# Kernel tuning notes

Hardware: AMD Instinct MI355X
Metric: run time of the kernel (lower is better)

The kernel has to match this reference:

```python
import jax, jax.numpy as jnp
import numpy as np

B = 131072
EPS = 1e-5

def _attn(x, Wq, Wk, Wv, Wo):
    # x: (B, 10, 1); Wq/Wk/Wv: (1, 16); Wo: (16, 1)
    Q = x @ Wq  # (B, 10, 16)
    K = x @ Wk
    V = x @ Wv
    A = jnp.einsum('bqd,bkd->bqk', Q, K) / 4.0  # sqrt(16) = 4
    A = jax.nn.softmax(A, axis=1)  # NOTE: torch Softmax(dim=1) -> axis 1, not -1
    out = jnp.einsum('bqk,bkd->bqd', A, V) @ Wo  # (B, 10, 1)
    return out[..., 0]  # squeeze -> (B, 10)

def _bn(h, gamma, beta):
    # BatchNorm1d training-mode math (batch stats, biased variance)
    mu = jnp.mean(h, axis=0)
    var = jnp.mean(jnp.square(h - mu), axis=0)
    return gamma * (h - mu) * jax.lax.rsqrt(var + EPS) + beta

def setup_inputs() -> dict:
    key = jax.random.key(0)
    ks = jax.random.split(key, 24)
    n = lambda k, shp, s=1.0: (jax.random.normal(k, shp, dtype=jnp.float32) * s)
    inp = {
        'x':   n(ks[0], (B, 10, 1)),
        'Wq1': n(ks[1], (1, 16)), 'Wk1': n(ks[2], (1, 16)),
        'Wv1': n(ks[3], (1, 16)), 'Wo1': n(ks[4], (16, 1)),
        'Wq2': n(ks[5], (1, 16)), 'Wk2': n(ks[6], (1, 16)),
        'Wv2': n(ks[7], (1, 16)), 'Wo2': n(ks[8], (16, 1)),
        # layer1: Linear(10,128) BN ReLU Linear(128,256) BN ReLU Linear(256,10)
        'W1a': n(ks[9], (10, 128), 0.3), 'b1a': jnp.zeros((128,), jnp.float32),
        'g1a': jnp.ones((128,), jnp.float32), 'be1a': jnp.zeros((128,), jnp.float32),
        'W1b': n(ks[10], (128, 256), 0.09), 'b1b': jnp.zeros((256,), jnp.float32),
        'g1b': jnp.ones((256,), jnp.float32), 'be1b': jnp.zeros((256,), jnp.float32),
        'W1c': n(ks[11], (256, 10), 0.06), 'b1c': jnp.zeros((10,), jnp.float32),
        # layer2: Linear(10,128) BN ReLU Linear(128,256) BN ReLU Linear(256,2)
        'W2a': n(ks[12], (10, 128), 0.3), 'b2a': jnp.zeros((128,), jnp.float32),
        'g2a': jnp.ones((128,), jnp.float32), 'be2a': jnp.zeros((128,), jnp.float32),
        'W2b': n(ks[13], (128, 256), 0.09), 'b2b': jnp.zeros((256,), jnp.float32),
        'g2b': jnp.ones((256,), jnp.float32), 'be2b': jnp.zeros((256,), jnp.float32),
        'W2c': n(ks[14], (256, 2), 0.06), 'b2c': jnp.zeros((2,), jnp.float32),
    }
    return inp

def reference(x, Wq1, Wk1, Wv1, Wo1, Wq2, Wk2, Wv2, Wo2,
              W1a, b1a, g1a, be1a, W1b, b1b, g1b, be1b, W1c, b1c,
              W2a, b2a, g2a, be2a, W2b, b2b, g2b, be2b, W2c, b2c):
    h = _attn(x, Wq1, Wk1, Wv1, Wo1)                 # (B, 10)
    h = jax.nn.relu(_bn(h @ W1a + b1a, g1a, be1a))   # (B, 128)
    h = jax.nn.relu(_bn(h @ W1b + b1b, g1b, be1b))   # (B, 256)
    h = h @ W1c + b1c                                # (B, 10)
    h = _attn(h[..., None], Wq2, Wk2, Wv2, Wo2)      # (B, 10)
    h = jax.nn.relu(_bn(h @ W2a + b2a, g2a, be2a))   # (B, 128)
    h = jax.nn.relu(_bn(h @ W2b + b2b, g2b, be2b))   # (B, 256)
    return h @ W2c + b2c                             # (B, 2)
```

## Files before the change

kernel.cpp:

```cpp
#include <hip/hip_runtime.h>
#include <hip/hip_bf16.h>

#define EPS 1e-5f
constexpr int BN = 131072;
constexpr int NBKT = 32;

typedef __attribute__((ext_vector_type(8))) short bf16x8;
typedef __attribute__((ext_vector_type(4))) float f32x4;

constexpr size_t OFF_H   = 0;
constexpr size_t OFF_HH  = OFF_H  + (size_t)BN*10;
constexpr size_t OFF_M1  = OFF_HH + (size_t)BN*10;
constexpr size_t OFF_S2  = OFF_M1 + 65;
constexpr size_t OFF_M3  = OFF_S2 + 512;
constexpr size_t OFF_S4  = OFF_M3 + 65;
constexpr size_t OFF_WA1 = OFF_S4 + 512;
constexpr size_t OFF_BA1 = OFF_WA1 + 1280;
constexpr size_t OFF_WA2 = OFF_BA1 + 128;
constexpr size_t OFF_BA2 = OFF_WA2 + 1280;
constexpr size_t OFF_SC2 = OFF_BA2 + 128;
constexpr size_t OFF_TC2 = OFF_SC2 + 256;
constexpr size_t OFF_SC4 = OFF_TC2 + 256;
constexpr size_t OFF_TC4 = OFF_SC4 + 256;
constexpr size_t OFF_WB1 = OFF_TC4 + 256;
constexpr size_t OFF_BB1 = OFF_WB1 + 32768;
constexpr size_t OFF_WB2 = OFF_BB1 + 256;
constexpr size_t OFF_BB2 = OFF_WB2 + 32768;
constexpr size_t OFF_P1  = OFF_BB2 + 256;
constexpr size_t OFF_P3  = OFF_P1 + 1024*65;
constexpr size_t OFF_S2B = OFF_P3 + 1024*65;
constexpr size_t OFF_S4B = OFF_S2B + (size_t)NBKT*512;
constexpr size_t OFF_WT1 = OFF_S4B + (size_t)NBKT*512;
constexpr size_t OFF_WT2 = OFF_WT1 + 16384;
constexpr size_t OFF_END = OFF_WT2 + 16384;
constexpr size_t OFF_Z_BYTES = ((OFF_END*4 + 255) & ~(size_t)255);
constexpr size_t WS_NEED = OFF_Z_BYTES + (size_t)256*BN*2;

__device__ __forceinline__ float wsum(float v){
  v += __shfl_down(v, 32);
  v += __shfl_down(v, 16);
  v += __shfl_down(v, 8);
  v += __shfl_down(v, 4);
  v += __shfl_down(v, 2);
  v += __shfl_down(v, 1);
  return v;
}

__device__ __forceinline__ unsigned pk_bf16(float a, float b){
  union { __hip_bfloat16 h[2]; unsigned u; } cv;
  cv.h[0] = __float2bfloat16(a);
  cv.h[1] = __float2bfloat16(b);
  return cv.u;
}

__device__ __forceinline__ unsigned short bf16_1(float a){
  union { __hip_bfloat16 h; unsigned short u; } cv;
  cv.h = __float2bfloat16(a);
  return cv.u;
}

__device__ __forceinline__ float bf16_to_f(unsigned short u){
  return __uint_as_float(((unsigned)u) << 16);
}

__device__ __forceinline__ void attn10(const float* xr, float cqk, float cvo, float* y){
  #pragma unroll
  for (int q=0;q<10;q++) y[q] = 0.f;
  #pragma unroll
  for (int k=0;k<10;k++){
    float t = cqk * xr[k];
    float m = t*xr[0];
    #pragma unroll
    for (int q=1;q<10;q++) m = fmaxf(m, t*xr[q]);
    float ex[10]; float s = 0.f;
    #pragma unroll
    for (int q=0;q<10;q++){ ex[q] = __expf(t*xr[q]-m); s += ex[q]; }
    float f = xr[k]/s;
    #pragma unroll
    for (int q=0;q<10;q++) y[q] += ex[q]*f;
  }
  #pragma unroll
  for (int q=0;q<10;q++) y[q] *= cvo;
}

__device__ __forceinline__ void moments_block(const float* y, float (*red)[65],
                                              float* Pb, int t){
  int lane = t & 63, w = t >> 6;
  #pragma unroll
  for (int i=0;i<10;i++){
    float v = wsum(y[i]);
    if (lane==0) red[w][i] = v;
  }
  #pragma unroll
  for (int i=0;i<10;i++){
    #pragma unroll
    for (int j=i;j<10;j++){
      float v = wsum(y[i]*y[j]);
      if (lane==0) red[w][10 + 10*i - i*(i-1)/2 + (j-i)] = v;
    }
  }
  __syncthreads();
  if (t < 65)
    Pb[(size_t)blockIdx.x*65 + t] = red[0][t]+red[1][t]+red[2][t]+red[3][t];
}

__device__ __forceinline__ void moments10(const float* y, float* M, int lane){
  #pragma unroll
  for (int i=0;i<10;i++){
    float s = wsum(y[i]);
    if (lane==0) atomicAdd(&M[i], s);
  }
  #pragma unroll
  for (int i=0;i<10;i++){
    #pragma unroll
    for (int j=i;j<10;j++){
      int id = 10*i - i*(i-1)/2 + (j-i);
      float s = wsum(y[i]*y[j]);
      if (lane==0) atomicAdd(&M[10+id], s);
    }
  }
}

__global__ __launch_bounds__(256) void k_attn_in(
    const float* __restrict__ x,
    const float* __restrict__ Wq, const float* __restrict__ Wk,
    const float* __restrict__ Wv, const float* __restrict__ Wo,
    float* __restrict__ h, float* __restrict__ Pb){
  __shared__ float xs[256][11];
  __shared__ float red[4][65];
  int t = threadIdx.x;
  size_t base = (size_t)blockIdx.x*2560;
  for (int idx=t; idx<2560; idx+=256) xs[idx/10][idx%10] = x[base+idx];
  float cqk=0.f, cvo=0.f;
  #pragma unroll
  for (int d=0;d<16;d++){ cqk += Wq[d]*Wk[d]; cvo += Wv[d]*Wo[d]; }
  cqk *= 0.25f;
  __syncthreads();
  float xr[10];
  #pragma unroll
  for (int q=0;q<10;q++) xr[q] = xs[t][q];
  float y[10];
  attn10(xr, cqk, cvo, y);
  #pragma unroll
  for (int q=0;q<10;q++) xs[t][q] = y[q];
  moments_block(y, red, Pb, t);
  for (int idx=t; idx<2560; idx+=256) h[base+idx] = xs[idx/10][idx%10];
}

__global__ void k_fold10_part(const float* __restrict__ Pb, int npart,
                              const float* __restrict__ W,
                              const float* __restrict__ bv, const float* __restrict__ g,
                              const float* __restrict__ be,
                              float* __restrict__ WT, float* __restrict__ bo){
  __shared__ float part[65][8];
  __shared__ float sM[65];
  int t = threadIdx.x;
  if (t < 520){
    int c = t>>3, k = t&7;
    int n = npart>>3;
    float acc = 0.f;
    #pragma unroll 4
    for (int i=0;i<n;i++) acc += Pb[(size_t)(k*n+i)*65 + c];
    part[c][k] = acc;
  }
  __syncthreads();
  if (t < 65){
    float a = 0.f;
    #pragma unroll
    for (int k=0;k<8;k++) a += part[t][k];
    sM[t] = a;
  }
  __syncthreads();
  int j = t;
  if (j >= 128) return;
  const float invB = 1.f/(float)BN;
  float Eh[10];
  #pragma unroll
  for (int i=0;i<10;i++) Eh[i] = sM[i]*invB;
  float wj[10];
  #pragma unroll
  for (int i=0;i<10;i++) wj[i] = W[i*128+j];
  float mu = bv[j];
  #pragma unroll
  for (int i=0;i<10;i++) mu += Eh[i]*wj[i];
  float var = 0.f;
  #pragma unroll
  for (int i=0;i<10;i++){
    #pragma unroll
    for (int l=0;l<10;l++){
      int a = i<l ? i : l, c = i<l ? l : i;
      int id = 10*a - a*(a-1)/2 + (c-a);
      float cov = sM[10+id]*invB - Eh[i]*Eh[l];
      var += wj[i]*wj[l]*cov;
    }
  }
  float s = g[j]*rsqrtf(var + EPS);
  #pragma unroll
  for (int i=0;i<10;i++) WT[j*10+i] = wj[i]*s;
  bo[j] = (bv[j]-mu)*s + be[j];
}

__global__ void k_fold10_atomic(const float* __restrict__ M,
                                const float* __restrict__ W,
                                const float* __restrict__ bv, const float* __restrict__ g,
                                const float* __restrict__ be,
                                float* __restrict__ WT, float* __restrict__ bo){
  int j = threadIdx.x;
  if (j >= 128) return;
  const float invB = 1.f/(float)BN;
  float Eh[10];
  #pragma unroll
  for (int i=0;i<10;i++) Eh[i] = M[i]*invB;
  float wj[10];
  #pragma unroll
  for (int i=0;i<10;i++) wj[i] = W[i*128+j];
  float mu = bv[j];
  #pragma unroll
  for (int i=0;i<10;i++) mu += Eh[i]*wj[i];
  float var = 0.f;
  #pragma unroll
  for (int i=0;i<10;i++){
    #pragma unroll
    for (int l=0;l<10;l++){
      int a = i<l ? i : l, c = i<l ? l : i;
      int id = 10*a - a*(a-1)/2 + (c-a);
      float cov = M[10+id]*invB - Eh[i]*Eh[l];
      var += wj[i]*wj[l]*cov;
    }
  }
  float s = g[j]*rsqrtf(var + EPS);
  #pragma unroll
  for (int i=0;i<10;i++) WT[j*10+i] = wj[i]*s;
  bo[j] = (bv[j]-mu)*s + be[j];
}

__global__ void k_fold_affine(const float* __restrict__ stats,
                              const float* __restrict__ g,
                              const float* __restrict__ be,
                              float* __restrict__ s, float* __restrict__ tt){
  int j = threadIdx.x;
  if (j >= 256) return;
  float su = 0.f, sq = 0.f;
  #pragma unroll 4
  for (int k=0;k<NBKT;k++){
    su += stats[k*512 + j];
    sq += stats[k*512 + 256 + j];
  }
  const float invB = 1.f/(float)BN;
  float mu  = su*invB;
  float var = sq*invB - mu*mu;
  float sc = g[j]*rsqrtf(var + EPS);
  s[j]  = sc;
  tt[j] = be[j] - mu*sc;
}

__global__ __launch_bounds__(256) void k_prep_wt2(
    const float* __restrict__ W1, const float* __restrict__ W2,
    unsigned short* __restrict__ WT1, unsigned short* __restrict__ WT2){
  int g = blockIdx.x;
  const float* W = (g < 128) ? W1 : W2;
  unsigned short* WT = (g < 128) ? WT1 : WT2;
  int idx = (g & 127)*256 + threadIdx.x;
  int c = idx >> 7, k = idx & 127;
  WT[idx] = bf16_1(W[k*256 + c]);
}

__device__ __forceinline__ void block_gemm(
    const float* __restrict__ h, const float* __restrict__ WaT,
    const float* __restrict__ ba, const unsigned short* __restrict__ WT,
    unsigned short* h1s, float (*hs)[11], float* sWaT,
    f32x4 (&acc)[4][4], int t, size_t row0)
{
  int lane = t & 63, w = t >> 6;
  int ci = lane & 15, g = lane >> 4;

  bf16x8 bfr[4][4];
  #pragma unroll
  for (int nt=0; nt<4; nt++)
    #pragma unroll
    for (int kt=0; kt<4; kt++){
      union { uint4 u; bf16x8 v; } cv;
      cv.u = *(const uint4*)(WT + (size_t)(w*64 + nt*16 + ci)*128 + kt*32 + g*8);
      bfr[nt][kt] = cv.v;
    }

  for (int idx = t; idx < 640; idx += 256) hs[idx/10][idx%10] = h[row0*10 + idx];
  for (int idx = t; idx < 1280; idx += 256) sWaT[idx] = WaT[idx];
  __syncthreads();

  {
    int r = lane;
    int i0 = w * 32;
    float hr[10];
    #pragma unroll
    for (int l=0;l<10;l++) hr[l] = hs[r][l];
    #pragma unroll
    for (int j=0;j<4;j++){
      unsigned pk[4];
      #pragma unroll
      for (int q=0;q<4;q++){
        int i = i0 + j*8 + q*2;
        float v0 = ba[i], v1 = ba[i+1];
        #pragma unroll
        for (int l=0;l<10;l++){
          v0 = fmaf(hr[l], sWaT[i*10+l],     v0);
          v1 = fmaf(hr[l], sWaT[(i+1)*10+l], v1);
        }
        pk[q] = pk_bf16(fmaxf(v0,0.f), fmaxf(v1,0.f));
      }
      int byte = r*256 + (((i0 + j*8)*2) ^ ((r&7)<<4));
      *(uint4*)((char*)h1s + byte) = make_uint4(pk[0],pk[1],pk[2],pk[3]);
    }
  }
  __syncthreads();

  #pragma unroll
  for (int mt=0;mt<4;mt++)
    #pragma unroll
    for (int nt=0;nt<4;nt++)
      acc[mt][nt] = (f32x4){0.f,0.f,0.f,0.f};

  #pragma unroll
  for (int mt=0; mt<4; mt++){
    int r = mt*16 + ci;
    bf16x8 af[4];
    #pragma unroll
    for (int kt=0; kt<4; kt++){
      int byte = r*256 + ((kt*64 + g*16) ^ ((r&7)<<4));
      af[kt] = *(const bf16x8*)((const char*)h1s + byte);
    }
    #pragma unroll
    for (int nt=0; nt<4; nt++)
      #pragma unroll
      for (int kt=0; kt<4; kt++)
        acc[mt][nt] = __builtin_amdgcn_mfma_f32_16x16x32_bf16(
            af[kt], bfr[nt][kt], acc[mt][nt], 0, 0, 0);
  }
}

__global__ __launch_bounds__(256) void k_layer_mfma(
    const float* __restrict__ h,
    const float* __restrict__ WaT,
    const float* __restrict__ ba,
    const unsigned short* __restrict__ WT,
    const float* __restrict__ bb,
    unsigned short* __restrict__ zt,
    float* __restrict__ stats)
{
  __shared__ __align__(16) char smem[36864];
  unsigned short* h1s = (unsigned short*)smem;
  float (*hs)[11]     = (float(*)[11])(smem + 16384);
  float* sWaT         = (float*)(smem + 19200);
  unsigned short* zs  = (unsigned short*)smem;
  int t = threadIdx.x;
  int lane = t & 63, w = t >> 6;
  int ci = lane & 15, g = lane >> 4;
  size_t row0 = (size_t)blockIdx.x * 64;

  f32x4 acc[4][4];
  block_gemm(h, WaT, ba, WT, h1s, hs, sWaT, acc, t, row0);

  float bbv[4];
  #pragma unroll
  for (int nt=0;nt<4;nt++) bbv[nt] = bb[w*64 + nt*16 + ci];
  float s1v[4], s2v[4];
  #pragma unroll
  for (int nt=0; nt<4; nt++){
    float cs = 0.f, cq = 0.f;
    #pragma unroll
    for (int mt=0; mt<4; mt++)
      #pragma unroll
      for (int j=0;j<4;j++){
        float zv = acc[mt][nt][j] + bbv[nt];
        acc[mt][nt][j] = zv;
        cs += zv;
        cq += zv*zv;
      }
    cs += __shfl_down(cs, 32); cs += __shfl_down(cs, 16);
    cq += __shfl_down(cq, 32); cq += __shfl_down(cq, 16);
    s1v[nt] = cs; s2v[nt] = cq;
  }
  __syncthreads();

  #pragma unroll
  for (int mt=0; mt<4; mt++)
    #pragma unroll
    for (int nt=0; nt<4; nt++){
      int c = w*64 + nt*16 + ci;
      int r0 = mt*16 + g*4;
      uint2 v;
      v.x = pk_bf16(acc[mt][nt][0], acc[mt][nt][1]);
      v.y = pk_bf16(acc[mt][nt][2], acc[mt][nt][3]);
      *(uint2*)&zs[c*72 + r0] = v;
    }
  __syncthreads();

  #pragma unroll
  for (int pass=0; pass<8; pass++){
    int c  = (t>>3) + pass*32;
    int rc = (t&7)*8;
    uint4 v = *(const uint4*)&zs[c*72 + rc];
    *(uint4*)(zt + (size_t)c*BN + row0 + rc) = v;
  }

  if (lane < 16){
    int bkt = blockIdx.x & (NBKT-1);
    #pragma unroll
    for (int nt=0; nt<4; nt++){
      int c = w*64 + nt*16 + ci;
      atomicAdd(&stats[bkt*512 + c],       s1v[nt]);
      atomicAdd(&stats[bkt*512 + 256 + c], s2v[nt]);
    }
  }
}

__global__ __launch_bounds__(256) void k_consume_mid(
    const unsigned short* __restrict__ zt,
    const float* __restrict__ s_g, const float* __restrict__ t_g,
    const float* __restrict__ Wc,  const float* __restrict__ bc,
    const float* __restrict__ Wq, const float* __restrict__ Wk,
    const float* __restrict__ Wv, const float* __restrict__ Wo,
    float* __restrict__ hh, float* __restrict__ Pb){
  __shared__ __align__(16) unsigned short zs[32*256];
  __shared__ __align__(16) float sWc[256*12];
  __shared__ float ss[256], st[256];
  __shared__ float red[4][65];
  int t = threadIdx.x;
  for (int idx=t; idx<2560; idx+=256) sWc[(idx/10)*12 + (idx%10)] = Wc[idx];
  ss[t] = s_g[t]; st[t] = t_g[t];
  size_t b0 = (size_t)blockIdx.x*256;

  float z3[10];
  #pragma unroll
  for (int l=0;l<10;l++) z3[l] = bc[l];

  int c8 = t >> 3, i8 = t & 7;
  for (int cc=0; cc<8; cc++){
    __syncthreads();
    {
      int c = cc*32 + c8;
      const uint4* src = (const uint4*)(zt + (size_t)c*BN + b0 + i8*32);
      uint4* dst = (uint4*)&zs[c8*256 + i8*32];
      dst[0] = src[0]; dst[1] = src[1]; dst[2] = src[2]; dst[3] = src[3];
    }
    __syncthreads();
    #pragma unroll 4
    for (int cl=0; cl<32; cl++){
      int c = cc*32 + cl;
      float f = bf16_to_f(zs[cl*256 + t]);
      float h2 = fmaxf(fmaf(ss[c], f, st[c]), 0.f);
      const float4* wr = (const float4*)&sWc[c*12];
      float4 w0 = wr[0];
      float4 w1 = wr[1];
      float2 w2 = *(const float2*)&sWc[c*12 + 8];
      z3[0] = fmaf(h2, w0.x, z3[0]); z3[1] = fmaf(h2, w0.y, z3[1]);
      z3[2] = fmaf(h2, w0.z, z3[2]); z3[3] = fmaf(h2, w0.w, z3[3]);
      z3[4] = fmaf(h2, w1.x, z3[4]); z3[5] = fmaf(h2, w1.y, z3[5]);
      z3[6] = fmaf(h2, w1.z, z3[6]); z3[7] = fmaf(h2, w1.w, z3[7]);
      z3[8] = fmaf(h2, w2.x, z3[8]); z3[9] = fmaf(h2, w2.y, z3[9]);
    }
  }

  float cqk=0.f, cvo=0.f;
  #pragma unroll
  for (int d=0;d<16;d++){ cqk += Wq[d]*Wk[d]; cvo += Wv[d]*Wo[d]; }
  cqk *= 0.25f;
  float y[10];
  attn10(z3, cqk, cvo, y);
  __syncthreads();
  float* hhs = (float*)zs;
  #pragma unroll
  for (int q=0;q<10;q++) hhs[t*10+q] = y[q];
  moments_block(y, red, Pb, t);
  for (int idx=t; idx<2560; idx+=256)
    hh[b0*10 + idx] = hhs[idx];
}

__global__ __launch_bounds__(256) void k_consume_out(
    const unsigned short* __restrict__ zt,
    const float* __restrict__ s_g, const float* __restrict__ t_g,
    const float* __restrict__ Wc,  const float* __restrict__ bc,
    float* __restrict__ out){
  __shared__ __align__(16) unsigned short zs[32*256];
  __shared__ __align__(8) float sWo[512];
  __shared__ float ss[256], st[256];
  int t = threadIdx.x;
  sWo[t] = Wc[t]; sWo[256+t] = Wc[256+t];
  ss[t] = s_g[t]; st[t] = t_g[t];
  size_t b0 = (size_t)blockIdx.x*256;
  float o0 = bc[0], o1 = bc[1];
  int c8 = t >> 3, i8 = t & 7;
  for (int cc=0; cc<8; cc++){
    __syncthreads();
    {
      int c = cc*32 + c8;
      const uint4* src = (const uint4*)(zt + (size_t)c*BN + b0 + i8*32);
      uint4* dst = (uint4*)&zs[c8*256 + i8*32];
      dst[0] = src[0]; dst[1] = src[1]; dst[2] = src[2]; dst[3] = src[3];
    }
    __syncthreads();
    #pragma unroll 8
    for (int cl=0; cl<32; cl++){
      int c = cc*32 + cl;
      float f = bf16_to_f(zs[cl*256 + t]);
      float h5 = fmaxf(fmaf(ss[c], f, st[c]), 0.f);
      float2 wv = *(const float2*)&sWo[c*2];
      o0 = fmaf(h5, wv.x, o0);
      o1 = fmaf(h5, wv.y, o1);
    }
  }
  *(float2*)(out + (b0 + t)*2) = make_float2(o0, o1);
}

__global__ void k_fold_big(const float* __restrict__ stats,
                           const float* __restrict__ W,
                           const float* __restrict__ bv, const float* __restrict__ g,
                           const float* __restrict__ be,
                           float* __restrict__ Wf, float* __restrict__ bf){
  int j = blockIdx.x*256 + threadIdx.x;
  if (j >= 256) return;
  const float invB = 1.f/(float)BN;
  float mu  = stats[j]*invB;
  float var = stats[256+j]*invB - mu*mu;
  float s = g[j]*rsqrtf(var + EPS);
  bf[j] = (bv[j]-mu)*s + be[j];
  for (int i=0;i<128;i++) Wf[i*256+j] = W[i*256+j]*s;
}

__global__ __launch_bounds__(256) void k_mid(
    const float* __restrict__ h,
    const float* __restrict__ WaT, const float* __restrict__ ba,
    const float* __restrict__ Wb,  const float* __restrict__ bb,
    float* __restrict__ stats){
  int b = blockIdx.x*256 + threadIdx.x;
  if (b >= BN) return;
  float hr[10];
  #pragma unroll
  for (int l=0;l<10;l++) hr[l] = h[(size_t)b*10+l];
  int lane = threadIdx.x & 63;
  for (int jc=0;jc<4;jc++){
    float acc[64];
    #pragma unroll
    for (int j=0;j<64;j++) acc[j] = bb[jc*64+j];
    for (int i=0;i<128;i++){
      float h1 = ba[i];
      #pragma unroll
      for (int l=0;l<10;l++) h1 += hr[l]*WaT[i*10+l];
      h1 = fmaxf(h1, 0.f);
      const float* __restrict__ w = &Wb[i*256 + jc*64];
      #pragma unroll
      for (int j=0;j<64;j++) acc[j] += h1*w[j];
    }
    #pragma unroll
    for (int j=0;j<64;j++){
      float s1 = wsum(acc[j]);
      float s2 = wsum(acc[j]*acc[j]);
      if (lane==0){
        atomicAdd(&stats[jc*64+j], s1);
        atomicAdd(&stats[256+jc*64+j], s2);
      }
    }
  }
}

__global__ __launch_bounds__(256) void k_mid2(
    const float* __restrict__ h,
    const float* __restrict__ WaT, const float* __restrict__ ba,
    const float* __restrict__ Wbf, const float* __restrict__ bbf,
    const float* __restrict__ Wc,  const float* __restrict__ bc,
    const float* __restrict__ Wq, const float* __restrict__ Wk,
    const float* __restrict__ Wv, const float* __restrict__ Wo,
    float* __restrict__ hh, float* __restrict__ M){
  int b = blockIdx.x*256 + threadIdx.x;
  if (b >= BN) return;
  float hr[10];
  #pragma unroll
  for (int l=0;l<10;l++) hr[l] = h[(size_t)b*10+l];
  float z3[10];
  #pragma unroll
  for (int l=0;l<10;l++) z3[l] = bc[l];
  for (int jc=0;jc<4;jc++){
    float acc[64];
    #pragma unroll
    for (int j=0;j<64;j++) acc[j] = bbf[jc*64+j];
    for (int i=0;i<128;i++){
      float h1 = ba[i];
      #pragma unroll
      for (int l=0;l<10;l++) h1 += hr[l]*WaT[i*10+l];
      h1 = fmaxf(h1, 0.f);
      const float* __restrict__ w = &Wbf[i*256 + jc*64];
      #pragma unroll
      for (int j=0;j<64;j++) acc[j] += h1*w[j];
    }
    #pragma unroll
    for (int j=0;j<64;j++){
      float h2 = fmaxf(acc[j], 0.f);
      const float* __restrict__ wc = &Wc[(jc*64+j)*10];
      #pragma unroll
      for (int l=0;l<10;l++) z3[l] += h2*wc[l];
    }
  }
  float cqk=0.f, cvo=0.f;
  #pragma unroll
  for (int d=0;d<16;d++){ cqk += Wq[d]*Wk[d]; cvo += Wv[d]*Wo[d]; }
  cqk *= 0.25f;
  float y[10];
  attn10(z3, cqk, cvo, y);
  #pragma unroll
  for (int q=0;q<10;q++) hh[(size_t)b*10+q] = y[q];
  moments10(y, M, threadIdx.x & 63);
}

__global__ __launch_bounds__(256) void k_out(
    const float* __restrict__ h,
    const float* __restrict__ WaT, const float* __restrict__ ba,
    const float* __restrict__ Wbf, const float* __restrict__ bbf,
    const float* __restrict__ Wc,  const float* __restrict__ bc,
    float* __restrict__ out){
  int b = blockIdx.x*256 + threadIdx.x;
  if (b >= BN) return;
  float hr[10];
  #pragma unroll
  for (int l=0;l<10;l++) hr[l] = h[(size_t)b*10+l];
  float o0 = bc[0], o1 = bc[1];
  for (int jc=0;jc<4;jc++){
    float acc[64];
    #pragma unroll
    for (int j=0;j<64;j++) acc[j] = bbf[jc*64+j];
    for (int i=0;i<128;i++){
      float h4 = ba[i];
      #pragma unroll
      for (int l=0;l<10;l++) h4 += hr[l]*WaT[i*10+l];
      h4 = fmaxf(h4, 0.f);
      const float* __restrict__ w = &Wbf[i*256 + jc*64];
      #pragma unroll
      for (int j=0;j<64;j++) acc[j] += h4*w[j];
    }
    #pragma unroll
    for (int j=0;j<64;j++){
      float h5 = fmaxf(acc[j], 0.f);
      o0 += h5*Wc[(jc*64+j)*2];
      o1 += h5*Wc[(jc*64+j)*2+1];
    }
  }
  out[(size_t)b*2]   = o0;
  out[(size_t)b*2+1] = o1;
}

extern "C" void kernel_launch(void* const* d_in, const int* in_sizes, int n_in,
                              void* d_out, int out_size, void* d_ws, size_t ws_size,
                              hipStream_t stream){
  const float* x   = (const float*)d_in[0];
  const float* Wq1 = (const float*)d_in[1];
  const float* Wk1 = (const float*)d_in[2];
  const float* Wv1 = (const float*)d_in[3];
  const float* Wo1 = (const float*)d_in[4];
  const float* Wq2 = (const float*)d_in[5];
  const float* Wk2 = (const float*)d_in[6];
  const float* Wv2 = (const float*)d_in[7];
  const float* Wo2 = (const float*)d_in[8];
  const float* W1a = (const float*)d_in[9];  const float* b1a = (const float*)d_in[10];
  const float* g1a = (const float*)d_in[11]; const float* be1a= (const float*)d_in[12];
  const float* W1b = (const float*)d_in[13]; const float* b1b = (const float*)d_in[14];
  const float* g1b = (const float*)d_in[15]; const float* be1b= (const float*)d_in[16];
  const float* W1c = (const float*)d_in[17]; const float* b1c = (const float*)d_in[18];
  const float* W2a = (const float*)d_in[19]; const float* b2a = (const float*)d_in[20];
  const float* g2a = (const float*)d_in[21]; const float* be2a= (const float*)d_in[22];
  const float* W2b = (const float*)d_in[23]; const float* b2b = (const float*)d_in[24];
  const float* g2b = (const float*)d_in[25]; const float* be2b= (const float*)d_in[26];
  const float* W2c = (const float*)d_in[27]; const float* b2c = (const float*)d_in[28];

  float* f   = (float*)d_ws;
  float* h   = f + OFF_H;
  float* hh  = f + OFF_HH;
  float* M1  = f + OFF_M1;
  float* S2  = f + OFF_S2;
  float* M3  = f + OFF_M3;
  float* S4  = f + OFF_S4;
  float* WA1 = f + OFF_WA1; float* BA1 = f + OFF_BA1;
  float* WA2 = f + OFF_WA2; float* BA2 = f + OFF_BA2;
  float* SC2 = f + OFF_SC2; float* TC2 = f + OFF_TC2;
  float* SC4 = f + OFF_SC4; float* TC4 = f + OFF_TC4;
  float* WB1 = f + OFF_WB1; float* BB1 = f + OFF_BB1;
  float* WB2 = f + OFF_WB2; float* BB2 = f + OFF_BB2;
  float* P1  = f + OFF_P1;  float* P3  = f + OFF_P3;
  float* S2B = f + OFF_S2B; float* S4B = f + OFF_S4B;
  unsigned short* WT1 = (unsigned short*)(f + OFF_WT1);
  unsigned short* WT2 = (unsigned short*)(f + OFF_WT2);
  unsigned short* ZT = (unsigned short*)((char*)d_ws + OFF_Z_BYTES);

  dim3 blk(256);
  dim3 grid256(BN/256);
  dim3 grid64(BN/64);

  if (ws_size >= WS_NEED){
    hipMemsetAsync(S2B, 0, (size_t)2*NBKT*512*sizeof(float), stream);
    k_prep_wt2<<<256,blk,0,stream>>>(W1b, W2b, WT1, WT2);
    k_attn_in<<<grid256,blk,0,stream>>>(x, Wq1,Wk1,Wv1,Wo1, h, P1);
    k_fold10_part<<<1,576,0,stream>>>(P1, 512, W1a,b1a,g1a,be1a, WA1,BA1);
    k_layer_mfma<<<grid64,blk,0,stream>>>(h, WA1,BA1, WT1,b1b, ZT, S2B);
    k_fold_affine<<<1,256,0,stream>>>(S2B, g1b, be1b, SC2, TC2);
    k_consume_mid<<<grid256,blk,0,stream>>>(ZT, SC2,TC2, W1c,b1c,
                                            Wq2,Wk2,Wv2,Wo2, hh, P3);
    k_fold10_part<<<1,576,0,stream>>>(P3, 512, W2a,b2a,g2a,be2a, WA2,BA2);
    k_layer_mfma<<<grid64,blk,0,stream>>>(hh, WA2,BA2, WT2,b2b, ZT, S4B);
    k_fold_affine<<<1,256,0,stream>>>(S4B, g2b, be2b, SC4, TC4);
    k_consume_out<<<grid256,blk,0,stream>>>(ZT, SC4,TC4, W2c,b2c, (float*)d_out);
  } else {
    hipMemsetAsync(M1, 0, (65+512+65+512)*sizeof(float), stream);
    k_attn_in<<<grid256,blk,0,stream>>>(x, Wq1,Wk1,Wv1,Wo1, h, P1);
    k_fold10_part<<<1,576,0,stream>>>(P1, 512, W1a,b1a,g1a,be1a, WA1,BA1);
    k_mid<<<grid256,blk,0,stream>>>(h, WA1,BA1, W1b,b1b, S2);
    k_fold_big<<<1,256,0,stream>>>(S2, W1b,b1b,g1b,be1b, WB1,BB1);
    k_mid2<<<grid256,blk,0,stream>>>(h, WA1,BA1, WB1,BB1, W1c,b1c,
                                     Wq2,Wk2,Wv2,Wo2, hh, M3);
    k_fold10_atomic<<<1,128,0,stream>>>(M3, W2a,b2a,g2a,be2a, WA2,BA2);
    k_mid<<<grid256,blk,0,stream>>>(hh, WA2,BA2, W2b,b2b, S4);
    k_fold_big<<<1,256,0,stream>>>(S4, W2b,b2b,g2b,be2b, WB2,BB2);
    k_out<<<grid256,blk,0,stream>>>(hh, WA2,BA2, WB2,BB2, W2c,b2c, (float*)d_out);
  }
}
```

Baseline: 218.5 us.

## Double-buffer z tile loads in consumer kernels and pad z row stride

The consumer kernels now prefetch the next 32-channel chunk of the transposed bf16 activation into registers while computing on the current chunk. The chunk is written into an alternate shared-memory buffer, which removes one barrier per iteration and overlaps global loads with FMA work. The z row stride is also padded from BN to BN+64 elements to avoid channel-aligned address aliasing across rows. The cost is doubled LDS use for zs and a slightly larger workspace, which may lower occupancy.

```diff
diff --git a/kernel.cpp b/kernel.cpp
--- a/kernel.cpp
+++ b/kernel.cpp
@@ -4,6 +4,7 @@
 #define EPS 1e-5f
 constexpr int BN = 131072;
 constexpr int NBKT = 32;
+constexpr int ZLD = BN + 64;
 
 typedef __attribute__((ext_vector_type(8))) short bf16x8;
 typedef __attribute__((ext_vector_type(4))) float f32x4;
@@ -34,7 +35,7 @@
 constexpr size_t OFF_WT2 = OFF_WT1 + 16384;
 constexpr size_t OFF_END = OFF_WT2 + 16384;
 constexpr size_t OFF_Z_BYTES = ((OFF_END*4 + 255) & ~(size_t)255);
-constexpr size_t WS_NEED = OFF_Z_BYTES + (size_t)256*BN*2;
+constexpr size_t WS_NEED = OFF_Z_BYTES + (size_t)256*ZLD*2;
 
 __device__ __forceinline__ float wsum(float v){
   v += __shfl_down(v, 32);
@@ -400,7 +401,7 @@
     int c  = (t>>3) + pass*32;
     int rc = (t&7)*8;
     uint4 v = *(const uint4*)&zs[c*72 + rc];
-    *(uint4*)(zt + (size_t)c*BN + row0 + rc) = v;
+    *(uint4*)(zt + (size_t)c*ZLD + row0 + rc) = v;
   }
 
   if (lane < 16){
@@ -421,7 +422,7 @@
     const float* __restrict__ Wq, const float* __restrict__ Wk,
     const float* __restrict__ Wv, const float* __restrict__ Wo,
     float* __restrict__ hh, float* __restrict__ Pb){
-  __shared__ __align__(16) unsigned short zs[32*256];
+  __shared__ __align__(16) unsigned short zs[2][32*256];
   __shared__ __align__(16) float sWc[256*12];
   __shared__ float ss[256], st[256];
   __shared__ float red[4][65];
@@ -435,19 +436,25 @@
   for (int l=0;l<10;l++) z3[l] = bc[l];
 
   int c8 = t >> 3, i8 = t & 7;
+  uint4 r0, r1, r2, r3;
+  {
+    const uint4* src = (const uint4*)(zt + (size_t)c8*ZLD + b0 + i8*32);
+    r0 = src[0]; r1 = src[1]; r2 = src[2]; r3 = src[3];
+    uint4* dst = (uint4*)&zs[0][c8*256 + i8*32];
+    dst[0] = r0; dst[1] = r1; dst[2] = r2; dst[3] = r3;
+  }
   for (int cc=0; cc<8; cc++){
     __syncthreads();
-    {
-      int c = cc*32 + c8;
-      const uint4* src = (const uint4*)(zt + (size_t)c*BN + b0 + i8*32);
-      uint4* dst = (uint4*)&zs[c8*256 + i8*32];
-      dst[0] = src[0]; dst[1] = src[1]; dst[2] = src[2]; dst[3] = src[3];
-    }
-    __syncthreads();
+    if (cc < 7){
+      int c = (cc+1)*32 + c8;
+      const uint4* src = (const uint4*)(zt + (size_t)c*ZLD + b0 + i8*32);
+      r0 = src[0]; r1 = src[1]; r2 = src[2]; r3 = src[3];
+    }
+    const unsigned short* zb = zs[cc&1];
     #pragma unroll 4
     for (int cl=0; cl<32; cl++){
       int c = cc*32 + cl;
-      float f = bf16_to_f(zs[cl*256 + t]);
+      float f = bf16_to_f(zb[cl*256 + t]);
       float h2 = fmaxf(fmaf(ss[c], f, st[c]), 0.f);
       const float4* wr = (const float4*)&sWc[c*12];
       float4 w0 = wr[0];
@@ -459,6 +466,10 @@
       z3[6] = fmaf(h2, w1.z, z3[6]); z3[7] = fmaf(h2, w1.w, z3[7]);
       z3[8] = fmaf(h2, w2.x, z3[8]); z3[9] = fmaf(h2, w2.y, z3[9]);
     }
+    if (cc < 7){
+      uint4* dst = (uint4*)&zs[(cc+1)&1][c8*256 + i8*32];
+      dst[0] = r0; dst[1] = r1; dst[2] = r2; dst[3] = r3;
+    }
   }
 
   float cqk=0.f, cvo=0.f;
@@ -468,7 +479,7 @@
   float y[10];
   attn10(z3, cqk, cvo, y);
   __syncthreads();
-  float* hhs = (float*)zs;
+  float* hhs = (float*)zs[0];
   #pragma unroll
   for (int q=0;q<10;q++) hhs[t*10+q] = y[q];
   moments_block(y, red, Pb, t);
@@ -481,7 +492,7 @@
     const float* __restrict__ s_g, const float* __restrict__ t_g,
     const float* __restrict__ Wc,  const float* __restrict__ bc,
     float* __restrict__ out){
-  __shared__ __align__(16) unsigned short zs[32*256];
+  __shared__ __align__(16) unsigned short zs[2][32*256];
   __shared__ __align__(8) float sWo[512];
   __shared__ float ss[256], st[256];
   int t = threadIdx.x;
@@ -490,23 +501,33 @@
   size_t b0 = (size_t)blockIdx.x*256;
   float o0 = bc[0], o1 = bc[1];
   int c8 = t >> 3, i8 = t & 7;
+  uint4 r0, r1, r2, r3;
+  {
+    const uint4* src = (const uint4*)(zt + (size_t)c8*ZLD + b0 + i8*32);
+    r0 = src[0]; r1 = src[1]; r2 = src[2]; r3 = src[3];
+    uint4* dst = (uint4*)&zs[0][c8*256 + i8*32];
+    dst[0] = r0; dst[1] = r1; dst[2] = r2; dst[3] = r3;
+  }
   for (int cc=0; cc<8; cc++){
     __syncthreads();
-    {
-      int c = cc*32 + c8;
-      const uint4* src = (const uint4*)(zt + (size_t)c*BN + b0 + i8*32);
-      uint4* dst = (uint4*)&zs[c8*256 + i8*32];
-      dst[0] = src[0]; dst[1] = src[1]; dst[2] = src[2]; dst[3] = src[3];
-    }
-    __syncthreads();
+    if (cc < 7){
+      int c = (cc+1)*32 + c8;
+      const uint4* src = (const uint4*)(zt + (size_t)c*ZLD + b0 + i8*32);
+      r0 = src[0]; r1 = src[1]; r2 = src[2]; r3 = src[3];
+    }
+    const unsigned short* zb = zs[cc&1];
     #pragma unroll 8
     for (int cl=0; cl<32; cl++){
       int c = cc*32 + cl;
-      float f = bf16_to_f(zs[cl*256 + t]);
+      float f = bf16_to_f(zb[cl*256 + t]);
       float h5 = fmaxf(fmaf(ss[c], f, st[c]), 0.f);
       float2 wv = *(const float2*)&sWo[c*2];
       o0 = fmaf(h5, wv.x, o0);
       o1 = fmaf(h5, wv.y, o1);
+    }
+    if (cc < 7){
+      uint4* dst = (uint4*)&zs[(cc+1)&1][c8*256 + i8*32];
+      dst[0] = r0; dst[1] = r1; dst[2] = r2; dst[3] = r3;
     }
   }
   *(float2*)(out + (b0 + t)*2) = make_float2(o0, o1);
```

Result: no change. 217.1 us (-0.6%).

## Store intermediate Z row-major and use MFMA for small output projections

Applied to the files above, without the earlier changes.

The layer kernel now writes the bf16 pre-BN activations row-major (B x 256) directly from accumulators instead of staging a transposed column-major layout through shared memory. The consume kernels switch to 64-row blocks that load contiguous rows into swizzled LDS, apply BN+ReLU in place, and compute the 256->10 and 256->2 projections with bf16 MFMA using pre-packed padded weights, produced by a new prep kernel. Partial moment buffers grow to match the larger grid. The direct scattered 2-byte global stores from the layer kernel may be poorly coalesced, and the projection inputs are now rounded to bf16.

```diff
diff --git a/kernel.cpp b/kernel.cpp
--- a/kernel.cpp
+++ b/kernel.cpp
@@ -27,14 +27,16 @@
 constexpr size_t OFF_WB2 = OFF_BB1 + 256;
 constexpr size_t OFF_BB2 = OFF_WB2 + 32768;
 constexpr size_t OFF_P1  = OFF_BB2 + 256;
-constexpr size_t OFF_P3  = OFF_P1 + 1024*65;
-constexpr size_t OFF_S2B = OFF_P3 + 1024*65;
+constexpr size_t OFF_P3  = OFF_P1 + 512*65;
+constexpr size_t OFF_S2B = OFF_P3 + (size_t)2048*65;
 constexpr size_t OFF_S4B = OFF_S2B + (size_t)NBKT*512;
 constexpr size_t OFF_WT1 = OFF_S4B + (size_t)NBKT*512;
 constexpr size_t OFF_WT2 = OFF_WT1 + 16384;
-constexpr size_t OFF_END = OFF_WT2 + 16384;
+constexpr size_t OFF_WCP = OFF_WT2 + 16384;
+constexpr size_t OFF_WOP = OFF_WCP + 2048;
+constexpr size_t OFF_END = OFF_WOP + 2048;
 constexpr size_t OFF_Z_BYTES = ((OFF_END*4 + 255) & ~(size_t)255);
-constexpr size_t WS_NEED = OFF_Z_BYTES + (size_t)256*BN*2;
+constexpr size_t WS_NEED = OFF_Z_BYTES + (size_t)BN*256*2;
 
 __device__ __forceinline__ float wsum(float v){
   v += __shfl_down(v, 32);
@@ -59,9 +61,8 @@
   return cv.u;
 }
 
-__device__ __forceinline__ float bf16_to_f(unsigned short u){
-  return __uint_as_float(((unsigned)u) << 16);
-}
+__device__ __forceinline__ float bf16_lo(unsigned u){ return __uint_as_float(u << 16); }
+__device__ __forceinline__ float bf16_hi(unsigned u){ return __uint_as_float(u & 0xffff0000u); }
 
 __device__ __forceinline__ void attn10(const float* xr, float cqk, float cvo, float* y){
   #pragma unroll
@@ -265,6 +266,20 @@
   WT[idx] = bf16_1(W[k*256 + c]);
 }
 
+__global__ void k_prep_wcp(const float* __restrict__ W1c, const float* __restrict__ W2c,
+                           unsigned short* __restrict__ WcP,
+                           unsigned short* __restrict__ WoP){
+  int t = threadIdx.x;
+  int lane = t & 63;
+  int q = lane & 15;
+  int kb = (t>>6)*32 + (lane>>4)*8;
+  #pragma unroll
+  for (int e=0;e<8;e++){
+    WcP[t*8+e] = (q<10) ? bf16_1(W1c[(kb+e)*10 + q]) : (unsigned short)0;
+    WoP[t*8+e] = (q<2)  ? bf16_1(W2c[(kb+e)*2  + q]) : (unsigned short)0;
+  }
+}
+
 __device__ __forceinline__ void block_gemm(
     const float* __restrict__ h, const float* __restrict__ WaT,
     const float* __restrict__ ba, const unsigned short* __restrict__ WT,
@@ -344,14 +359,12 @@
     const float* __restrict__ ba,
     const unsigned short* __restrict__ WT,
     const float* __restrict__ bb,
-    unsigned short* __restrict__ zt,
+    unsigned short* __restrict__ z,
     float* __restrict__ stats)
 {
-  __shared__ __align__(16) char smem[36864];
-  unsigned short* h1s = (unsigned short*)smem;
-  float (*hs)[11]     = (float(*)[11])(smem + 16384);
-  float* sWaT         = (float*)(smem + 19200);
-  unsigned short* zs  = (unsigned short*)smem;
+  __shared__ unsigned short h1s[64*128];
+  __shared__ float hs[64][11];
+  __shared__ float sWaT[1280];
   int t = threadIdx.x;
   int lane = t & 63, w = t >> 6;
   int ci = lane & 15, g = lane >> 4;
@@ -367,12 +380,14 @@
   #pragma unroll
   for (int nt=0; nt<4; nt++){
     float cs = 0.f, cq = 0.f;
+    int c = w*64 + nt*16 + ci;
     #pragma unroll
     for (int mt=0; mt<4; mt++)
       #pragma unroll
       for (int j=0;j<4;j++){
         float zv = acc[mt][nt][j] + bbv[nt];
-        acc[mt][nt][j] = zv;
+        int r = mt*16 + g*4 + j;
+        z[(row0 + r)*256 + c] = bf16_1(zv);
         cs += zv;
         cq += zv*zv;
       }
@@ -380,29 +395,6 @@
     cq += __shfl_down(cq, 32); cq += __shfl_down(cq, 16);
     s1v[nt] = cs; s2v[nt] = cq;
   }
-  __syncthreads();
-
-  #pragma unroll
-  for (int mt=0; mt<4; mt++)
-    #pragma unroll
-    for (int nt=0; nt<4; nt++){
-      int c = w*64 + nt*16 + ci;
-      int r0 = mt*16 + g*4;
-      uint2 v;
-      v.x = pk_bf16(acc[mt][nt][0], acc[mt][nt][1]);
-      v.y = pk_bf16(acc[mt][nt][2], acc[mt][nt][3]);
-      *(uint2*)&zs[c*72 + r0] = v;
-    }
-  __syncthreads();
-
-  #pragma unroll
-  for (int pass=0; pass<8; pass++){
-    int c  = (t>>3) + pass*32;
-    int rc = (t&7)*8;
-    uint4 v = *(const uint4*)&zs[c*72 + rc];
-    *(uint4*)(zt + (size_t)c*BN + row0 + rc) = v;
-  }
-
   if (lane < 16){
     int bkt = blockIdx.x & (NBKT-1);
     #pragma unroll
@@ -415,101 +407,196 @@
 }
 
 __global__ __launch_bounds__(256) void k_consume_mid(
-    const unsigned short* __restrict__ zt,
+    const unsigned short* __restrict__ z,
     const float* __restrict__ s_g, const float* __restrict__ t_g,
-    const float* __restrict__ Wc,  const float* __restrict__ bc,
+    const unsigned short* __restrict__ WcP, const float* __restrict__ bc,
     const float* __restrict__ Wq, const float* __restrict__ Wk,
     const float* __restrict__ Wv, const float* __restrict__ Wo,
     float* __restrict__ hh, float* __restrict__ Pb){
-  __shared__ __align__(16) unsigned short zs[32*256];
-  __shared__ __align__(16) float sWc[256*12];
+  __shared__ __align__(16) unsigned short zs[64*256];
   __shared__ float ss[256], st[256];
-  __shared__ float red[4][65];
+  __shared__ float z3s[64][10];
   int t = threadIdx.x;
-  for (int idx=t; idx<2560; idx+=256) sWc[(idx/10)*12 + (idx%10)] = Wc[idx];
+  int lane = t & 63, w = t >> 6;
+  int ci = lane & 15, g = lane >> 4;
+  size_t row0 = (size_t)blockIdx.x * 64;
+
   ss[t] = s_g[t]; st[t] = t_g[t];
-  size_t b0 = (size_t)blockIdx.x*256;
-
-  float z3[10];
-  #pragma unroll
-  for (int l=0;l<10;l++) z3[l] = bc[l];
-
-  int c8 = t >> 3, i8 = t & 7;
-  for (int cc=0; cc<8; cc++){
-    __syncthreads();
-    {
-      int c = cc*32 + c8;
-      const uint4* src = (const uint4*)(zt + (size_t)c*BN + b0 + i8*32);
-      uint4* dst = (uint4*)&zs[c8*256 + i8*32];
-      dst[0] = src[0]; dst[1] = src[1]; dst[2] = src[2]; dst[3] = src[3];
-    }
-    __syncthreads();
-    #pragma unroll 4
-    for (int cl=0; cl<32; cl++){
-      int c = cc*32 + cl;
-      float f = bf16_to_f(zs[cl*256 + t]);
-      float h2 = fmaxf(fmaf(ss[c], f, st[c]), 0.f);
-      const float4* wr = (const float4*)&sWc[c*12];
-      float4 w0 = wr[0];
-      float4 w1 = wr[1];
-      float2 w2 = *(const float2*)&sWc[c*12 + 8];
-      z3[0] = fmaf(h2, w0.x, z3[0]); z3[1] = fmaf(h2, w0.y, z3[1]);
-      z3[2] = fmaf(h2, w0.z, z3[2]); z3[3] = fmaf(h2, w0.w, z3[3]);
-      z3[4] = fmaf(h2, w1.x, z3[4]); z3[5] = fmaf(h2, w1.y, z3[5]);
-      z3[6] = fmaf(h2, w1.z, z3[6]); z3[7] = fmaf(h2, w1.w, z3[7]);
-      z3[8] = fmaf(h2, w2.x, z3[8]); z3[9] = fmaf(h2, w2.y, z3[9]);
-    }
-  }
-
+
+  bf16x8 bfr[8];
+  #pragma unroll
+  for (int kt=0; kt<8; kt++){
+    union { uint4 u; bf16x8 v; } cv;
+    cv.u = ((const uint4*)WcP)[kt*64 + lane];
+    bfr[kt] = cv.v;
+  }
+
+  const uint4* zg = (const uint4*)(z + row0*256);
+  #pragma unroll
+  for (int p=0; p<8; p++){
+    int li = p*256 + t;
+    int r  = li >> 5;
+    int ck = (li & 31) ^ (r & 7);
+    *(uint4*)((char*)zs + r*512 + ck*16) = zg[li];
+  }
+  __syncthreads();
+
+  {
+    int r = t >> 2;
+    int ck0 = (t & 3) * 8;
+    #pragma unroll
+    for (int k=0; k<8; k++){
+      int ck = ck0 + k;
+      int c0 = ck * 8;
+      char* p = (char*)zs + r*512 + ((ck ^ (r&7))*16);
+      uint4 v = *(uint4*)p;
+      float4 s0 = *(const float4*)&ss[c0];
+      float4 s1 = *(const float4*)&ss[c0+4];
+      float4 t0 = *(const float4*)&st[c0];
+      float4 t1 = *(const float4*)&st[c0+4];
+      float h0 = fmaxf(fmaf(s0.x, bf16_lo(v.x), t0.x), 0.f);
+      float h1 = fmaxf(fmaf(s0.y, bf16_hi(v.x), t0.y), 0.f);
+      float h2 = fmaxf(fmaf(s0.z, bf16_lo(v.y), t0.z), 0.f);
+      float h3 = fmaxf(fmaf(s0.w, bf16_hi(v.y), t0.w), 0.f);
+      float h4 = fmaxf(fmaf(s1.x, bf16_lo(v.z), t1.x), 0.f);
+      float h5 = fmaxf(fmaf(s1.y, bf16_hi(v.z), t1.y), 0.f);
+      float h6 = fmaxf(fmaf(s1.z, bf16_lo(v.w), t1.z), 0.f);
+      float h7 = fmaxf(fmaf(s1.w, bf16_hi(v.w), t1.w), 0.f);
+      *(uint4*)p = make_uint4(pk_bf16(h0,h1), pk_bf16(h2,h3),
+                              pk_bf16(h4,h5), pk_bf16(h6,h7));
+    }
+  }
+  __syncthreads();
+
+  f32x4 acc = (f32x4){0.f,0.f,0.f,0.f};
+  {
+    int r = w*16 + ci;
+    #pragma unroll
+    for (int kt=0; kt<8; kt++){
+      int ck = (kt*4 + g) ^ (r & 7);
+      bf16x8 af = *(const bf16x8*)((const char*)zs + r*512 + ck*16);
+      acc = __builtin_amdgcn_mfma_f32_16x16x32_bf16(af, bfr[kt], acc, 0, 0, 0);
+    }
+  }
+  if (ci < 10){
+    #pragma unroll
+    for (int j=0;j<4;j++) z3s[w*16 + g*4 + j][ci] = acc[j];
+  }
+  __syncthreads();
+
+  float* red = (float*)zs;
+  float* hhs = (float*)zs + 256;
   float cqk=0.f, cvo=0.f;
   #pragma unroll
   for (int d=0;d<16;d++){ cqk += Wq[d]*Wk[d]; cvo += Wv[d]*Wo[d]; }
   cqk *= 0.25f;
-  float y[10];
-  attn10(z3, cqk, cvo, y);
-  __syncthreads();
-  float* hhs = (float*)zs;
-  #pragma unroll
-  for (int q=0;q<10;q++) hhs[t*10+q] = y[q];
-  moments_block(y, red, Pb, t);
-  for (int idx=t; idx<2560; idx+=256)
-    hh[b0*10 + idx] = hhs[idx];
+
+  if (t < 64){
+    float z3[10];
+    #pragma unroll
+    for (int l=0;l<10;l++) z3[l] = bc[l] + z3s[t][l];
+    float y[10];
+    attn10(z3, cqk, cvo, y);
+    #pragma unroll
+    for (int q=0;q<10;q++) hhs[t*10+q] = y[q];
+    #pragma unroll
+    for (int i=0;i<10;i++){
+      float v = wsum(y[i]);
+      if (lane==0) red[i] = v;
+    }
+    #pragma unroll
+    for (int i=0;i<10;i++){
+      #pragma unroll
+      for (int j=i;j<10;j++){
+        float v = wsum(y[i]*y[j]);
+        if (lane==0) red[10 + 10*i - i*(i-1)/2 + (j-i)] = v;
+      }
+    }
+  }
+  __syncthreads();
+  if (t < 65) Pb[(size_t)blockIdx.x*65 + t] = red[t];
+  for (int idx=t; idx<640; idx+=256) hh[row0*10 + idx] = hhs[idx];
 }
 
 __global__ __launch_bounds__(256) void k_consume_out(
-    const unsigned short* __restrict__ zt,
+    const unsigned short* __restrict__ z,
     const float* __restrict__ s_g, const float* __restrict__ t_g,
-    const float* __restrict__ Wc,  const float* __restrict__ bc,
+    const unsigned short* __restrict__ WoP, const float* __restrict__ bc,
     float* __restrict__ out){
-  __shared__ __align__(16) unsigned short zs[32*256];
-  __shared__ __align__(8) float sWo[512];
+  __shared__ __align__(16) unsigned short zs[64*256];
   __shared__ float ss[256], st[256];
+  __shared__ float o_s[64][2];
   int t = threadIdx.x;
-  sWo[t] = Wc[t]; sWo[256+t] = Wc[256+t];
+  int lane = t & 63, w = t >> 6;
+  int ci = lane & 15, g = lane >> 4;
+  size_t row0 = (size_t)blockIdx.x * 64;
+
   ss[t] = s_g[t]; st[t] = t_g[t];
-  size_t b0 = (size_t)blockIdx.x*256;
-  float o0 = bc[0], o1 = bc[1];
-  int c8 = t >> 3, i8 = t & 7;
-  for (int cc=0; cc<8; cc++){
-    __syncthreads();
-    {
-      int c = cc*32 + c8;
-      const uint4* src = (const uint4*)(zt + (size_t)c*BN + b0 + i8*32);
-      uint4* dst = (uint4*)&zs[c8*256 + i8*32];
-      dst[0] = src[0]; dst[1] = src[1]; dst[2] = src[2]; dst[3] = src[3];
-    }
-    __syncthreads();
-    #pragma unroll 8
-    for (int cl=0; cl<32; cl++){
-      int c = cc*32 + cl;
-      float f = bf16_to_f(zs[cl*256 + t]);
-      float h5 = fmaxf(fmaf(ss[c], f, st[c]), 0.f);
-      float2 wv = *(const float2*)&sWo[c*2];
-      o0 = fmaf(h5, wv.x, o0);
-      o1 = fmaf(h5, wv.y, o1);
-    }
-  }
-  *(float2*)(out + (b0 + t)*2) = make_float2(o0, o1);
+
+  bf16x8 bfr[8];
+  #pragma unroll
+  for (int kt=0; kt<8; kt++){
+    union { uint4 u; bf16x8 v; } cv;
+    cv.u = ((const uint4*)WoP)[kt*64 + lane];
+    bfr[kt] = cv.v;
+  }
+
+  const uint4* zg = (const uint4*)(z + row0*256);
+  #pragma unroll
+  for (int p=0; p<8; p++){
+    int li = p*256 + t;
+    int r  = li >> 5;
+    int ck = (li & 31) ^ (r & 7);
+    *(uint4*)((char*)zs + r*512 + ck*16) = zg[li];
+  }
+  __syncthreads();
+
+  {
+    int r = t >> 2;
+    int ck0 = (t & 3) * 8;
+    #pragma unroll
+    for (int k=0; k<8; k++){
+      int ck = ck0 + k;
+      int c0 = ck * 8;
+      char* p = (char*)zs + r*512 + ((ck ^ (r&7))*16);
+      uint4 v = *(uint4*)p;
+      float4 s0 = *(const float4*)&ss[c0];
+      float4 s1 = *(const float4*)&ss[c0+4];
+      float4 t0 = *(const float4*)&st[c0];
+      float4 t1 = *(const float4*)&st[c0+4];
+      float h0 = fmaxf(fmaf(s0.x, bf16_lo(v.x), t0.x), 0.f);
+      float h1 = fmaxf(fmaf(s0.y, bf16_hi(v.x), t0.y), 0.f);
+      float h2 = fmaxf(fmaf(s0.z, bf16_lo(v.y), t0.z), 0.f);
+      float h3 = fmaxf(fmaf(s0.w, bf16_hi(v.y), t0.w), 0.f);
+      float h4 = fmaxf(fmaf(s1.x, bf16_lo(v.z), t1.x), 0.f);
+      float h5 = fmaxf(fmaf(s1.y, bf16_hi(v.z), t1.y), 0.f);
+      float h6 = fmaxf(fmaf(s1.z, bf16_lo(v.w), t1.z), 0.f);
+      float h7 = fmaxf(fmaf(s1.w, bf16_hi(v.w), t1.w), 0.f);
+      *(uint4*)p = make_uint4(pk_bf16(h0,h1), pk_bf16(h2,h3),
+                              pk_bf16(h4,h5), pk_bf16(h6,h7));
+    }
+  }
+  __syncthreads();
+
+  f32x4 acc = (f32x4){0.f,0.f,0.f,0.f};
+  {
+    int r = w*16 + ci;
+    #pragma unroll
+    for (int kt=0; kt<8; kt++){
+      int ck = (kt*4 + g) ^ (r & 7);
+      bf16x8 af = *(const bf16x8*)((const char*)zs + r*512 + ck*16);
+      acc = __builtin_amdgcn_mfma_f32_16x16x32_bf16(af, bfr[kt], acc, 0, 0, 0);
+    }
+  }
+  if (ci < 2){
+    #pragma unroll
+    for (int j=0;j<4;j++) o_s[w*16 + g*4 + j][ci] = acc[j];
+  }
+  __syncthreads();
+  if (t < 64){
+    *(float2*)(out + (row0 + t)*2) = make_float2(bc[0] + o_s[t][0],
+                                                 bc[1] + o_s[t][1]);
+  }
 }
 
 __global__ void k_fold_big(const float* __restrict__ stats,
@@ -687,7 +774,9 @@
   float* S2B = f + OFF_S2B; float* S4B = f + OFF_S4B;
   unsigned short* WT1 = (unsigned short*)(f + OFF_WT1);
   unsigned short* WT2 = (unsigned short*)(f + OFF_WT2);
-  unsigned short* ZT = (unsigned short*)((char*)d_ws + OFF_Z_BYTES);
+  unsigned short* WCP = (unsigned short*)(f + OFF_WCP);
+  unsigned short* WOP = (unsigned short*)(f + OFF_WOP);
+  unsigned short* Z  = (unsigned short*)((char*)d_ws + OFF_Z_BYTES);
 
   dim3 blk(256);
   dim3 grid256(BN/256);
@@ -696,16 +785,17 @@
   if (ws_size >= WS_NEED){
     hipMemsetAsync(S2B, 0, (size_t)2*NBKT*512*sizeof(float), stream);
     k_prep_wt2<<<256,blk,0,stream>>>(W1b, W2b, WT1, WT2);
+    k_prep_wcp<<<1,512,0,stream>>>(W1c, W2c, WCP, WOP);
     k_attn_in<<<grid256,blk,0,stream>>>(x, Wq1,Wk1,Wv1,Wo1, h, P1);
     k_fold10_part<<<1,576,0,stream>>>(P1, 512, W1a,b1a,g1a,be1a, WA1,BA1);
-    k_layer_mfma<<<grid64,blk,0,stream>>>(h, WA1,BA1, WT1,b1b, ZT, S2B);
+    k_layer_mfma<<<grid64,blk,0,stream>>>(h, WA1,BA1, WT1,b1b, Z, S2B);
     k_fold_affine<<<1,256,0,stream>>>(S2B, g1b, be1b, SC2, TC2);
-    k_consume_mid<<<grid256,blk,0,stream>>>(ZT, SC2,TC2, W1c,b1c,
-                                            Wq2,Wk2,Wv2,Wo2, hh, P3);
-    k_fold10_part<<<1,576,0,stream>>>(P3, 512, W2a,b2a,g2a,be2a, WA2,BA2);
-    k_layer_mfma<<<grid64,blk,0,stream>>>(hh, WA2,BA2, WT2,b2b, ZT, S4B);
+    k_consume_mid<<<grid64,blk,0,stream>>>(Z, SC2,TC2, WCP,b1c,
+                                           Wq2,Wk2,Wv2,Wo2, hh, P3);
+    k_fold10_part<<<1,576,0,stream>>>(P3, 2048, W2a,b2a,g2a,be2a, WA2,BA2);
+    k_layer_mfma<<<grid64,blk,0,stream>>>(hh, WA2,BA2, WT2,b2b, Z, S4B);
     k_fold_affine<<<1,256,0,stream>>>(S4B, g2b, be2b, SC4, TC4);
-    k_consume_out<<<grid256,blk,0,stream>>>(ZT, SC4,TC4, W2c,b2c, (float*)d_out);
+    k_consume_out<<<grid64,blk,0,stream>>>(Z, SC4,TC4, WOP,b2c, (float*)d_out);
   } else {
     hipMemsetAsync(M1, 0, (65+512+65+512)*sizeof(float), stream);
     k_attn_in<<<grid256,blk,0,stream>>>(x, Wq1,Wk1,Wv1,Wo1, h, P1);
```

New measurement: 266.3 us. +21.9%, slower.
